# Performance work log

Hardware: AMD Instinct MI355X
Metric: run time of the kernel (lower is better)

The kernel has to match this reference:

```python
import jax, jax.numpy as jnp
import numpy as np

KS_LIST = (7, 9, 11)
DILS = (1, 2, 4, 8, 16, 32)
PER = 5          # kernels per (kernel_size, dilation) group
EPS = 1e-5       # BatchNorm1d eps
N, C, L = 512, 12, 8192


def _rocket_features(x, W7, b7, W9, b9, W11, b11):
    # x: [N, C, L]; W_ks: [6*PER, C, ks]; b_ks: [6*PER]
    dn = ('NCH', 'OIH', 'NCH')
    feats = []
    for W, b in ((W7, b7), (W9, b9), (W11, b11)):
        for j, d in enumerate(DILS):
            w = W[j * PER:(j + 1) * PER]      # [PER, C, ks]
            bb = b[j * PER:(j + 1) * PER]     # [PER]
            # one dilated conv for all PER kernels in this group -> [N, PER, L]
            out = jax.lax.conv_general_dilated(
                x, w, window_strides=(1,), padding='SAME',
                rhs_dilation=(d,), dimension_numbers=dn) + bb[None, :, None]
            ppv = jnp.mean((out > 0).astype(x.dtype), axis=2)  # [N, PER]
            mx = jnp.max(out, axis=2)                          # [N, PER]
            # interleave (ppv_k, max_k) per kernel, matching the torch loop order
            feats.append(jnp.stack([ppv, mx], axis=-1).reshape(x.shape[0], 2 * PER))
    f = jnp.concatenate(feats, axis=1)  # [N, 2*nb_kernels] = [N, 180]
    # BatchNorm1d(affine=False), training mode: batch stats, biased variance
    mean = jnp.mean(f, axis=0)
    var = jnp.var(f, axis=0)
    return (f - mean) / jnp.sqrt(var + EPS)


def setup_inputs() -> dict:
    key = jax.random.key(0)
    kx, k1, k2, k3, k4, k5, k6 = jax.random.split(key, 7)
    G = len(DILS) * PER  # 30 kernels per kernel-size family
    inp = {
        'x': jax.random.normal(kx, (N, C, L), dtype=jnp.float32),
        'W7': jax.random.uniform(k1, (G, C, 7), minval=-1.0, maxval=1.0, dtype=jnp.float32),
        'b7': jax.random.normal(k2, (G,), dtype=jnp.float32),
        'W9': jax.random.uniform(k3, (G, C, 9), minval=-1.0, maxval=1.0, dtype=jnp.float32),
        'b9': jax.random.normal(k4, (G,), dtype=jnp.float32),
        'W11': jax.random.uniform(k5, (G, C, 11), minval=-1.0, maxval=1.0, dtype=jnp.float32),
        'b11': jax.random.normal(k6, (G,), dtype=jnp.float32),
    }
    return inp


def reference(x, W7, b7, W9, b9, W11, b11):
    return _rocket_features(x, W7, b7, W9, b9, W11, b11)
```

## Files before the change

### kernel.cpp

```cpp
#include <hip/hip_runtime.h>
#include <math.h>
#include <limits.h>

#define N_SAMP 512
#define C_IN   12
#define L_IN   8192
#define NDIL   6
#define NFILT  30
#define NFEAT  180
#define NCHUNK 4
#define CHUNK  (L_IN / NCHUNK)
#define EPSV   1e-5f

#define HALO   160
#define TLC    512
#define LWC    (TLC + 2*HALO)
#define TILEB  (LWC * 16)

#define WF_OFF (3 * N_SAMP * NCHUNK * NFILT * 2)
#define WTAB_B (NDIL * 3 * 64 * 16)

typedef __attribute__((ext_vector_type(4))) int i32x4;

__device__ __forceinline__ int swz(int r) {
    return (r << 4) ^ ((((r >> 3) ^ (r >> 6)) & 7) << 4);
}

__global__ __launch_bounds__(256)
void build_wb(const float* __restrict__ W7, const float* __restrict__ W9,
              const float* __restrict__ W11, const float* __restrict__ b7,
              const float* __restrict__ b9, const float* __restrict__ b11,
              signed char* __restrict__ wc, signed char* __restrict__ wd,
              float* __restrict__ bias_tab)
{
    const int t = blockIdx.x * 256 + threadIdx.x;
    if (t < NDIL * 3 * 64) {
        const int j    = t / 192;
        const int mf   = (t / 64) % 3;
        const int lane = t % 64;
        const int col  = lane & 15;
        const int q    = lane >> 4;
        const int tap  = mf * 4 + q;
#pragma unroll
        for (int e = 0; e < 16; ++e) {
            float v = 0.0f;
            if (col < 15 && tap <= 10 && e < 12) {
                const int toff = tap - 5;
                if (col < 5) {
                    if (toff >= -3 && toff <= 3)
                        v = W7[((j * 5 + col) * 12 + e) * 7 + toff + 3];
                } else if (col < 10) {
                    if (toff >= -4 && toff <= 4)
                        v = W9[((j * 5 + col - 5) * 12 + e) * 9 + toff + 4];
                } else {
                    v = W11[((j * 5 + col - 10) * 12 + e) * 11 + toff + 5];
                }
            }
            const int W  = __float2int_rn(v * 8192.0f);
            const int C8 = (W + 128) >> 8;
            const int D8 = W - (C8 << 8);
            wc[(size_t)t * 16 + e] = (signed char)C8;
            wd[(size_t)t * 16 + e] = (signed char)D8;
        }
    } else if (t < NDIL * 3 * 64 + 96) {
        const int i = t - NDIL * 3 * 64;
        const int j = i / 16, s = i % 16;
        float b = 0.0f;
        if (s < 5)       b = b7 [j * 5 + s];
        else if (s < 10) b = b9 [j * 5 + s - 5];
        else if (s < 15) b = b11[j * 5 + s - 10];
        bias_tab[j * 16 + s] = b;
    }
}

__global__ __launch_bounds__(256)
void rocket_conv_i8(const float* __restrict__ x,
                    const signed char* __restrict__ wc,
                    const signed char* __restrict__ wd,
                    const float* __restrict__ bias_tab,
                    float* __restrict__ ws)
{
    __shared__ __align__(16) signed char xq[2][TILEB];
    __shared__ int redcnt[4 * NDIL * 16];
    __shared__ int redmx [4 * NDIL * 16];

    const int ch  = blockIdx.x;
    const int n   = blockIdx.y;
    const int tid = threadIdx.x;
    const int lane = tid & 63, wv = tid >> 6;
    const int row_l = lane & 15, q = lane >> 4;
    const float* __restrict__ xrow = x + (size_t)n * C_IN * L_IN;
    const i32x4* __restrict__ wcv = (const i32x4*)wc;
    const i32x4* __restrict__ wdv = (const i32x4*)wd;

    for (int i = tid; i < 4 * NDIL * 16; i += 256) {
        redcnt[i] = 0;
        redmx[i]  = INT_MIN;
    }

    const int c0 = ch * CHUNK;
#pragma unroll 1
    for (int st = 0; st < CHUNK / TLC; ++st) {
        const int t0 = c0 + st * TLC;
        __syncthreads();
#pragma unroll 1
        for (int r = tid; r < LWC; r += 256) {
            const int g = t0 - HALO + r;
            int h[4] = {0, 0, 0, 0}, l[4] = {0, 0, 0, 0};
            if ((unsigned)g < (unsigned)L_IN) {
#pragma unroll
                for (int c = 0; c < 12; ++c) {
                    const float xv = xrow[c * L_IN + g];
                    const int X  = __float2int_rn(xv * 4096.0f);
                    const int A8 = (X + 128) >> 8;
                    const int B8 = X - (A8 << 8);
                    h[c >> 2] |= (A8 & 255) << ((c & 3) * 8);
                    l[c >> 2] |= (B8 & 255) << ((c & 3) * 8);
                }
            }
            const int cell = swz(r);
            *(i32x4*)&xq[0][cell] = (i32x4){h[0], h[1], h[2], h[3]};
            *(i32x4*)&xq[1][cell] = (i32x4){l[0], l[1], l[2], l[3]};
        }
        __syncthreads();

#pragma unroll 1
        for (int j = 0; j < NDIL; ++j) {
            const int d = 1 << j;
            const i32x4 C0 = wcv[(j * 3 + 0) * 64 + lane];
            const i32x4 C1 = wcv[(j * 3 + 1) * 64 + lane];
            const i32x4 C2 = wcv[(j * 3 + 2) * 64 + lane];
            const i32x4 D0 = wdv[(j * 3 + 0) * 64 + lane];
            const i32x4 D1 = wdv[(j * 3 + 1) * 64 + lane];
            const i32x4 D2 = wdv[(j * 3 + 2) * 64 + lane];
            const float bj = bias_tab[j * 16 + row_l];
            const int tj = (int)floorf(bj * -33554432.0f);
            const int r0 = HALO + wv * 128 + row_l + (q - 5) * d;
            const int r1 = HALO + wv * 128 + row_l + (q - 1) * d;
            const int r2 = HALO + wv * 128 + row_l +
                           ((q == 3) ? 0 : (q + 3) * d);

            int cnt_i = 0, mx_i = INT_MIN;
#pragma unroll
            for (int t = 0; t < 8; ++t) {
                const int cell0 = swz(r0 + 16 * t);
                const int cell1 = swz(r1 + 16 * t);
                const int cell2 = swz(r2 + 16 * t);
                i32x4 a0 = {0, 0, 0, 0};
                i32x4 a1 = {0, 0, 0, 0};
                i32x4 a2 = {0, 0, 0, 0};
                {
                    i32x4 ah = *(const i32x4*)&xq[0][cell0];
                    i32x4 al = *(const i32x4*)&xq[1][cell0];
                    a0 = __builtin_amdgcn_mfma_i32_16x16x64_i8(ah, C0, a0, 0, 0, 0);
                    a1 = __builtin_amdgcn_mfma_i32_16x16x64_i8(ah, D0, a1, 0, 0, 0);
                    a1 = __builtin_amdgcn_mfma_i32_16x16x64_i8(al, C0, a1, 0, 0, 0);
                    a2 = __builtin_amdgcn_mfma_i32_16x16x64_i8(al, D0, a2, 0, 0, 0);
                }
                {
                    i32x4 ah = *(const i32x4*)&xq[0][cell1];
                    i32x4 al = *(const i32x4*)&xq[1][cell1];
                    a0 = __builtin_amdgcn_mfma_i32_16x16x64_i8(ah, C1, a0, 0, 0, 0);
                    a1 = __builtin_amdgcn_mfma_i32_16x16x64_i8(ah, D1, a1, 0, 0, 0);
                    a1 = __builtin_amdgcn_mfma_i32_16x16x64_i8(al, C1, a1, 0, 0, 0);
                    a2 = __builtin_amdgcn_mfma_i32_16x16x64_i8(al, D1, a2, 0, 0, 0);
                }
                {
                    i32x4 ah = *(const i32x4*)&xq[0][cell2];
                    i32x4 al = *(const i32x4*)&xq[1][cell2];
                    a0 = __builtin_amdgcn_mfma_i32_16x16x64_i8(ah, C2, a0, 0, 0, 0);
                    a1 = __builtin_amdgcn_mfma_i32_16x16x64_i8(ah, D2, a1, 0, 0, 0);
                    a1 = __builtin_amdgcn_mfma_i32_16x16x64_i8(al, C2, a1, 0, 0, 0);
                    a2 = __builtin_amdgcn_mfma_i32_16x16x64_i8(al, D2, a2, 0, 0, 0);
                }
#pragma unroll
                for (int i = 0; i < 4; ++i) {
                    const int tot = (a0[i] << 16) + (a1[i] << 8) + a2[i];
                    cnt_i += (tot > tj) ? 1 : 0;
                    mx_i   = (tot > mx_i) ? tot : mx_i;
                }
            }

            cnt_i += __shfl_xor(cnt_i, 16);
            cnt_i += __shfl_xor(cnt_i, 32);
            {
                int o = __shfl_xor(mx_i, 16);  mx_i = (o > mx_i) ? o : mx_i;
                o     = __shfl_xor(mx_i, 32);  mx_i = (o > mx_i) ? o : mx_i;
            }
            if (lane < 16) {
                const int idx = (wv * NDIL + j) * 16 + lane;
                redcnt[idx] += cnt_i;
                if (mx_i > redmx[idx]) redmx[idx] = mx_i;
            }
        }
    }

    __syncthreads();
    if (tid < 96) {
        const int jj = tid >> 4, s = tid & 15;
        if (s < 15) {
            int c = 0, m = INT_MIN;
#pragma unroll
            for (int w = 0; w < 4; ++w) {
                c += redcnt[(w * NDIL + jj) * 16 + s];
                const int v = redmx[(w * NDIL + jj) * 16 + s];
                m = (v > m) ? v : m;
            }
            const float bj = bias_tab[jj * 16 + s];
            const int ks = s / 5, f = s % 5;
            const int gg = jj * 5 + f;
            const size_t base =
                ((((size_t)ks * N_SAMP + n) * NCHUNK + ch) * NFILT + gg) * 2;
            ws[base]     = (float)c;
            ws[base + 1] = bj + (float)m * 2.9802322387695312e-8f;
        }
    }
}

__global__ __launch_bounds__(512)
void rocket_finish(const float* __restrict__ ws, float* __restrict__ out)
{
    const int i = blockIdx.x;
    const int t = threadIdx.x;

    const int ks = i / 60;
    const int r  = i % 60;
    const int g  = r >> 1;
    const int m  = r & 1;

    const size_t base =
        ((((size_t)ks * N_SAMP + t) * NCHUNK) * NFILT + g) * 2 + m;

    float v;
    if (m) {
        v = -INFINITY;
#pragma unroll
        for (int c = 0; c < NCHUNK; ++c)
            v = fmaxf(v, ws[base + (size_t)c * NFILT * 2]);
    } else {
        v = 0.0f;
#pragma unroll
        for (int c = 0; c < NCHUNK; ++c)
            v += ws[base + (size_t)c * NFILT * 2];
        v *= (1.0f / (float)L_IN);
    }

    float s  = v;
    float sq = v * v;
#pragma unroll
    for (int off = 32; off; off >>= 1) {
        s  += __shfl_xor(s, off);
        sq += __shfl_xor(sq, off);
    }

    __shared__ float ss[8], sqq[8];
    const int lane = t & 63;
    const int wv   = t >> 6;
    if (lane == 0) { ss[wv] = s; sqq[wv] = sq; }
    __syncthreads();
    if (t == 0) {
        float S = 0.0f, Q = 0.0f;
#pragma unroll
        for (int w = 0; w < 8; ++w) { S += ss[w]; Q += sqq[w]; }
        ss[0] = S; sqq[0] = Q;
    }
    __syncthreads();

    const float mean = ss[0] * (1.0f / (float)N_SAMP);
    const float var  = sqq[0] * (1.0f / (float)N_SAMP) - mean * mean;
    out[t * NFEAT + i] = (v - mean) / sqrtf(var + EPSV);
}

extern "C" void kernel_launch(void* const* d_in, const int* in_sizes, int n_in,
                              void* d_out, int out_size, void* d_ws, size_t ws_size,
                              hipStream_t stream)
{
    const float* x   = (const float*)d_in[0];
    const float* W7  = (const float*)d_in[1];
    const float* b7  = (const float*)d_in[2];
    const float* W9  = (const float*)d_in[3];
    const float* b9  = (const float*)d_in[4];
    const float* W11 = (const float*)d_in[5];
    const float* b11 = (const float*)d_in[6];
    float* out = (float*)d_out;
    float* ws  = (float*)d_ws;
    signed char* wc = (signed char*)(ws + WF_OFF);
    signed char* wd = wc + WTAB_B;
    float* bias_tab = (float*)(wd + WTAB_B);

    build_wb<<<5, 256, 0, stream>>>(W7, W9, W11, b7, b9, b11, wc, wd, bias_tab);

    dim3 grid(NCHUNK, N_SAMP);
    rocket_conv_i8<<<grid, 256, 0, stream>>>(x, wc, wd, bias_tab, ws);

    rocket_finish<<<NFEAT, 512, 0, stream>>>(ws, out);
}
```

Before: 286.2 us.

## Shrink time tile to 256 and reduce per-block stats with LDS atomics

Halves the time tile per stage (TLC 512→256), so each wave covers 64 outputs per dilation and the LDS footprint drops. The aim is to fit more blocks per CU and hide the quantize/load phase. The cost is that the fixed halo of 160 on each side is now large relative to the tile, so redundant halo quantization and global reads roughly double in proportion. The per-wave reduction arrays are replaced by shared atomicAdd/atomicMax into one slot per filter, and the epilogue max/count is tree-reduced.

```diff
diff --git a/kernel.cpp b/kernel.cpp
--- a/kernel.cpp
+++ b/kernel.cpp
@@ -13,7 +13,7 @@
 #define EPSV   1e-5f
 
 #define HALO   160
-#define TLC    512
+#define TLC    256
 #define LWC    (TLC + 2*HALO)
 #define TILEB  (LWC * 16)
 
@@ -81,8 +81,8 @@
                     float* __restrict__ ws)
 {
     __shared__ __align__(16) signed char xq[2][TILEB];
-    __shared__ int redcnt[4 * NDIL * 16];
-    __shared__ int redmx [4 * NDIL * 16];
+    __shared__ int scnt[NDIL * 16];
+    __shared__ int smx [NDIL * 16];
 
     const int ch  = blockIdx.x;
     const int n   = blockIdx.y;
@@ -93,9 +93,9 @@
     const i32x4* __restrict__ wcv = (const i32x4*)wc;
     const i32x4* __restrict__ wdv = (const i32x4*)wd;
 
-    for (int i = tid; i < 4 * NDIL * 16; i += 256) {
-        redcnt[i] = 0;
-        redmx[i]  = INT_MIN;
+    if (tid < NDIL * 16) {
+        scnt[tid] = 0;
+        smx[tid]  = INT_MIN;
     }
 
     const int c0 = ch * CHUNK;
@@ -135,14 +135,14 @@
             const i32x4 D2 = wdv[(j * 3 + 2) * 64 + lane];
             const float bj = bias_tab[j * 16 + row_l];
             const int tj = (int)floorf(bj * -33554432.0f);
-            const int r0 = HALO + wv * 128 + row_l + (q - 5) * d;
-            const int r1 = HALO + wv * 128 + row_l + (q - 1) * d;
-            const int r2 = HALO + wv * 128 + row_l +
+            const int r0 = HALO + wv * 64 + row_l + (q - 5) * d;
+            const int r1 = HALO + wv * 64 + row_l + (q - 1) * d;
+            const int r2 = HALO + wv * 64 + row_l +
                            ((q == 3) ? 0 : (q + 3) * d);
 
             int cnt_i = 0, mx_i = INT_MIN;
 #pragma unroll
-            for (int t = 0; t < 8; ++t) {
+            for (int t = 0; t < 4; ++t) {
                 const int cell0 = swz(r0 + 16 * t);
                 const int cell1 = swz(r1 + 16 * t);
                 const int cell2 = swz(r2 + 16 * t);
@@ -173,12 +173,18 @@
                     a1 = __builtin_amdgcn_mfma_i32_16x16x64_i8(al, C2, a1, 0, 0, 0);
                     a2 = __builtin_amdgcn_mfma_i32_16x16x64_i8(al, D2, a2, 0, 0, 0);
                 }
-#pragma unroll
-                for (int i = 0; i < 4; ++i) {
-                    const int tot = (a0[i] << 16) + (a1[i] << 8) + a2[i];
-                    cnt_i += (tot > tj) ? 1 : 0;
-                    mx_i   = (tot > mx_i) ? tot : mx_i;
-                }
+                int t01, t23;
+                {
+                    const int v0 = (a0[0] << 16) + (a1[0] << 8) + a2[0];
+                    const int v1 = (a0[1] << 16) + (a1[1] << 8) + a2[1];
+                    const int v2 = (a0[2] << 16) + (a1[2] << 8) + a2[2];
+                    const int v3 = (a0[3] << 16) + (a1[3] << 8) + a2[3];
+                    cnt_i += (v0 > tj) + (v1 > tj) + (v2 > tj) + (v3 > tj);
+                    t01 = (v0 > v1) ? v0 : v1;
+                    t23 = (v2 > v3) ? v2 : v3;
+                }
+                const int tmx = (t01 > t23) ? t01 : t23;
+                mx_i = (tmx > mx_i) ? tmx : mx_i;
             }
 
             cnt_i += __shfl_xor(cnt_i, 16);
@@ -188,9 +194,8 @@
                 o     = __shfl_xor(mx_i, 32);  mx_i = (o > mx_i) ? o : mx_i;
             }
             if (lane < 16) {
-                const int idx = (wv * NDIL + j) * 16 + lane;
-                redcnt[idx] += cnt_i;
-                if (mx_i > redmx[idx]) redmx[idx] = mx_i;
+                atomicAdd(&scnt[j * 16 + lane], cnt_i);
+                atomicMax(&smx[j * 16 + lane], mx_i);
             }
         }
     }
@@ -199,13 +204,8 @@
     if (tid < 96) {
         const int jj = tid >> 4, s = tid & 15;
         if (s < 15) {
-            int c = 0, m = INT_MIN;
-#pragma unroll
-            for (int w = 0; w < 4; ++w) {
-                c += redcnt[(w * NDIL + jj) * 16 + s];
-                const int v = redmx[(w * NDIL + jj) * 16 + s];
-                m = (v > m) ? v : m;
-            }
+            const int c = scnt[jj * 16 + s];
+            const int m = smx[jj * 16 + s];
             const float bj = bias_tab[jj * 16 + s];
             const int ks = s / 5, f = s % 5;
             const int gg = jj * 5 + f;
```

New measurement: 300.8 us. 1.05x slower.
